# Kernel tuning notes

Hardware: AMD Instinct MI355X
Metric: run time of the kernel (lower is better)

## Reference

```python
import jax, jax.numpy as jnp
import numpy as np

N_NODES = 50000
N_EDGES = 400000
N_GRAPHS = 512
F = 32        # num_features
NB = 32       # mp_num_basis_fn
ZMAX = 118
CUTOFF = 5.0
NSPH = 9      # (mp_max_degree+1)^2 with max_degree=2
DEG_IDX = jnp.array([0, 1, 1, 1, 2, 2, 2, 2, 2])  # degree of each spherical component


def _bernstein(u, n=NB):
    # reciprocal_bernstein radial basis: Bernstein polynomials of degree n-1 at u in [0,1)
    k = jnp.arange(n, dtype=jnp.float32)
    log_binom = (jax.scipy.special.gammaln(float(n)) - jax.scipy.special.gammaln(k + 1.0)
                 - jax.scipy.special.gammaln(float(n) - k))
    u = jnp.clip(u, 1e-7, 1.0 - 1e-7)[..., None]
    return jnp.exp(log_binom + k * jnp.log(u) + (float(n) - 1.0 - k) * jnp.log1p(-u))


def _smooth_cutoff(r, cutoff=CUTOFF):
    t = r / cutoff
    return jnp.where(t < 1.0, jnp.exp(1.0 - 1.0 / jnp.clip(1.0 - t * t, 1e-7, None)), 0.0)


def _sph(u):
    # real spherical harmonics (cartesian normalization) up to degree 2; u: (E,3) unit vectors
    x, y, z = u[:, 0], u[:, 1], u[:, 2]
    c = jnp.sqrt(jnp.float32(3.0))
    return jnp.stack([jnp.ones_like(x), y, z, x,
                      c * x * y, c * y * z, 0.5 * (3.0 * z * z - 1.0),
                      c * z * x, 0.5 * c * (x * x - y * y)], axis=-1)


def _dense(x, W, b):
    # equivariant Dense: shared kernel over spherical components, bias only on scalar (l=0)
    y = jnp.einsum('nmf,fg->nmg', x, W)
    return y.at[:, 0, :].add(b)


def _silu_gate(x):
    # equivariant silu: scalar channel gates all degrees (scalar part -> exact silu)
    return x * jax.nn.sigmoid(x[:, 0:1, :])


def setup_inputs() -> dict:
    key = jax.random.key(0)
    ks = jax.random.split(key, 24)
    s = 1.0 / np.sqrt(F)
    sb = 1.0 / np.sqrt(NB)
    inp = {
        'positions': 2.0 * jax.random.normal(ks[0], (N_NODES, 3), jnp.float32),
        'embed': jax.random.normal(ks[1], (ZMAX, F), jnp.float32),
        'Wy0': sb * jax.random.normal(ks[2], (3, NB, F), jnp.float32),
        'Wx0': sb * jax.random.normal(ks[3], (3, NB, F), jnp.float32),
        'W1_0': s * jax.random.normal(ks[4], (F, F), jnp.float32),
        'b1_0': jnp.zeros((F,), jnp.float32),
        'W2_0': s * jax.random.normal(ks[5], (F, F), jnp.float32),
        'b2_0': jnp.zeros((F,), jnp.float32),
        'c0': jnp.full((1,), 0.5, jnp.float32),
        'Wr_last': sb * jax.random.normal(ks[6], (NB, F), jnp.float32),
        'W1_1': s * jax.random.normal(ks[7], (F, F), jnp.float32),
        'b1_1': jnp.zeros((F,), jnp.float32),
        'W2_1': s * jax.random.normal(ks[8], (F, F), jnp.float32),
        'b2_1': jnp.zeros((F,), jnp.float32),
        'c1': jnp.full((1,), 0.5, jnp.float32),
        'Wro1': s * jax.random.normal(ks[9], (F, F), jnp.float32),
        'bro1': jnp.zeros((F,), jnp.float32),
        'Wro2': s * jax.random.normal(ks[10], (F, 1), jnp.float32),
        'bro2': jnp.zeros((1,), jnp.float32),
        'atomic_bias': jax.random.normal(ks[11], (ZMAX,), jnp.float32),
        'atomic_numbers': jax.random.randint(ks[12], (N_NODES,), 0, ZMAX, jnp.int32),
        'dst_idx': jax.random.randint(ks[13], (N_EDGES,), 0, N_NODES, jnp.int32),
        'src_idx': jax.random.randint(ks[14], (N_EDGES,), 0, N_NODES, jnp.int32),
        'batch_segments': jnp.sort(jax.random.randint(ks[15], (N_NODES,), 0, N_GRAPHS, jnp.int32)),
        'graph_mask': jnp.ones((N_GRAPHS,), jnp.bool_),
    }
    return inp


def reference(positions, embed, Wy0, Wx0, W1_0, b1_0, W2_0, b2_0, c0,
              Wr_last, W1_1, b1_1, W2_1, b2_1, c1,
              Wro1, bro1, Wro2, bro2, atomic_bias,
              atomic_numbers, dst_idx, src_idx, batch_segments, graph_mask):
    # --- edge geometry (gather_src/gather_dst) ---
    disp = positions[src_idx] - positions[dst_idx]                # (E,3)
    r = jnp.sqrt(jnp.sum(disp * disp, axis=-1) + 1e-12)           # (E,)
    u = disp / r[:, None]
    Y = _sph(u)                                                   # (E,9)
    rbf = _bernstein(r / (r + 1.0)) * _smooth_cutoff(r)[:, None]  # (E,NB)

    # --- atomic embedding, lifted to (N, 9, F) with zero higher degrees ---
    x0 = embed[atomic_numbers]                                    # (N,F)
    x = jnp.concatenate([x0[:, None, :], jnp.zeros((N_NODES, NSPH - 1, F), x0.dtype)], axis=1)

    # --- iteration 0: full-degree equivariant message pass ---
    wy = jnp.einsum('eb,lbf->elf', rbf, Wy0)[:, DEG_IDX, :]       # (E,9,F) radial weights, (0,l)->l path
    wx = jnp.einsum('eb,lbf->elf', rbf, Wx0)[:, DEG_IDX, :]       # (l,0)->l path
    xs = x[src_idx]                                               # (E,9,F)
    msg = wy * Y[:, :, None] * xs[:, 0:1, :] + wx * xs
    y = jax.ops.segment_sum(msg, dst_idx, num_segments=N_NODES)   # (N,9,F)
    y = x + y
    y = _silu_gate(_dense(y, W1_0, b1_0))
    y = _dense(y, W2_0, b2_0)
    x = x + jax.nn.silu(c0) * y                                   # y_nl == 0 (era disabled)

    # --- iteration 1 (last): max_degree=0 message pass, then reduce to scalars ---
    w0 = rbf @ Wr_last                                            # (E,F)
    msg0 = w0 * x[src_idx, 0, :]
    y0 = jax.ops.segment_sum(msg0, dst_idx, num_segments=N_NODES) # (N,F)
    xs0 = x[:, 0, :]                                              # change_max_degree -> scalars
    y0 = xs0 + y0
    y0 = jax.nn.silu(y0 @ W1_1 + b1_1)
    y0 = y0 @ W2_1 + b2_1
    xs0 = xs0 + jax.nn.silu(c1) * y0

    # --- atomic readout and per-graph sum ---
    h = jax.nn.silu(xs0 @ Wro1 + bro1)
    e_atom = (h @ Wro2)[:, 0] + bro2[0] + atomic_bias[atomic_numbers]
    e_graph = jax.ops.segment_sum(e_atom, batch_segments, num_segments=N_GRAPHS)
    return jnp.where(graph_mask, e_graph, 0.0)
```

## Files before the change

### kernel.cpp

```cpp
#include <hip/hip_runtime.h>
#include <math.h>

#define NNODES 50000
#define NEDGES 400000
#define NGRAPHS 512
#define FDIM 32
#define CAP 32

#define NHALVES 4096
#define NPAIRS (NNODES / 2)
#define PQ   (NPAIRS / NHALVES)
#define PREM (NPAIRS % NHALVES)

static constexpr float BINOM31[32] = {
    1.f, 31.f, 465.f, 4495.f, 31465.f, 169911.f, 736281.f, 2629575.f,
    7888725.f, 20160075.f, 44352165.f, 84672315.f, 141120525.f, 206253075.f,
    265182525.f, 300540195.f, 300540195.f, 265182525.f, 206253075.f,
    141120525.f, 84672315.f, 44352165.f, 20160075.f, 7888725.f, 2629575.f,
    736281.f, 169911.f, 31465.f, 4495.f, 465.f, 31.f, 1.f
};

__device__ __forceinline__ float fast_rcp(float x) {
    return __builtin_amdgcn_rcpf(x);
}
__device__ __forceinline__ float silu(float x) {
    return x * fast_rcp(1.0f + __expf(-x));
}

__global__ __launch_bounds__(256) void build_csr(
    const float* __restrict__ pos,
    const int* __restrict__ srci, const int* __restrict__ dsti,
    const int* __restrict__ Z,
    float4* __restrict__ pay, int* __restrict__ deg,
    float* __restrict__ out)
{
    int e = blockIdx.x * 256 + threadIdx.x;
    if (e < NGRAPHS) out[e] = 0.0f;
    if (e >= NEDGES) return;
    int s = srci[e], d = dsti[e];
    float dx = pos[3 * s]     - pos[3 * d];
    float dy = pos[3 * s + 1] - pos[3 * d + 1];
    float dz = pos[3 * s + 2] - pos[3 * d + 2];
    float r = sqrtf(dx * dx + dy * dy + dz * dz + 1e-12f);
    if (r >= 5.0f) return;

    float t = r * 0.2f;
    float q = fmaxf(1.0f - t * t, 1e-7f);
    float cut = __expf(1.0f - fast_rcp(q));
    float v = fast_rcp(r + 1.0f);
    float v2 = v * v, v4 = v2 * v2, v8 = v4 * v4, v16 = v8 * v8;
    float scale = v16 * v8 * v4 * v2 * v * cut;

    int rank = atomicAdd(&deg[d], 1);
    if (rank < CAP)
        pay[(size_t)d * CAP + rank] =
            make_float4(r, scale,
                        __int_as_float(s * FDIM),
                        __int_as_float(Z[s] * FDIM));
}

#define GATHER4X2(ACCA, ACCB, XSRC, SEL)                                   \
    float ACCA = 0.0f, ACCB = 0.0f;                                        \
    {                                                                      \
        int _dm = max(dgA, dgB);                                           \
        for (int j = 0; j < _dm; j += 4) {                                 \
            float rrA[4], scA[4], xgA[4], hhA[4];                          \
            float rrB[4], scB[4], xgB[4], hhB[4];                          \
            _Pragma("unroll")                                              \
            for (int k = 0; k < 4; ++k) {                                  \
                float4 _pA = plA[j + k];                                   \
                float4 _pB = plB[j + k];                                   \
                rrA[k] = _pA.x; scA[k] = _pA.y;                            \
                rrB[k] = _pB.x; scB[k] = _pB.y;                            \
                xgA[k] = (XSRC)[__float_as_int(_pA.SEL) + f];              \
                xgB[k] = (XSRC)[__float_as_int(_pB.SEL) + f];              \
            }                                                              \
            _Pragma("unroll")                                              \
            for (int k = 0; k < 4; ++k) { hhA[k] = cw[31]; hhB[k] = cw[31]; } \
            _Pragma("unroll")                                              \
            for (int t = 30; t >= 0; --t) {                                \
                _Pragma("unroll")                                          \
                for (int k = 0; k < 4; ++k) {                              \
                    hhA[k] = fmaf(hhA[k], rrA[k], cw[t]);                  \
                    hhB[k] = fmaf(hhB[k], rrB[k], cw[t]);                  \
                }                                                          \
            }                                                              \
            _Pragma("unroll")                                              \
            for (int k = 0; k < 4; ++k) {                                  \
                ACCA = fmaf(scA[k] * hhA[k], xgA[k], ACCA);                \
                ACCB = fmaf(scB[k] * hhB[k], xgB[k], ACCB);                \
            }                                                              \
        }                                                                  \
    }

#define MV2C(AA, AB, WR, YPA, YPB, c)                                      \
    { float4 _qA = (YPA)[c]; float4 _qB = (YPB)[c];                        \
      AA = fmaf(_qA.x, WR[4*c],   AA); AB = fmaf(_qB.x, WR[4*c],   AB);    \
      AA = fmaf(_qA.y, WR[4*c+1], AA); AB = fmaf(_qB.y, WR[4*c+1], AB);    \
      AA = fmaf(_qA.z, WR[4*c+2], AA); AB = fmaf(_qB.z, WR[4*c+2], AB);    \
      AA = fmaf(_qA.w, WR[4*c+3], AA); AB = fmaf(_qB.w, WR[4*c+3], AB); }

#define MATVEC32R2(RA, RB, WR, BIAS, YPA, YPB) do {                        \
    float _aA0=(BIAS), _aA1=0.f, _aA2=0.f, _aA3=0.f;                       \
    float _aB0=(BIAS), _aB1=0.f, _aB2=0.f, _aB3=0.f;                       \
    MV2C(_aA0,_aB0,WR,YPA,YPB,0) MV2C(_aA1,_aB1,WR,YPA,YPB,1)              \
    MV2C(_aA2,_aB2,WR,YPA,YPB,2) MV2C(_aA3,_aB3,WR,YPA,YPB,3)              \
    MV2C(_aA0,_aB0,WR,YPA,YPB,4) MV2C(_aA1,_aB1,WR,YPA,YPB,5)              \
    MV2C(_aA2,_aB2,WR,YPA,YPB,6) MV2C(_aA3,_aB3,WR,YPA,YPB,7)              \
    RA = (_aA0+_aA1)+(_aA2+_aA3);                                          \
    RB = (_aB0+_aB1)+(_aB2+_aB3); } while (0)

__device__ __forceinline__ void pair_range(int h, int& p0, int& p1) {
    int a = h < PREM ? h * (PQ + 1) : PREM * (PQ + 1) + (h - PREM) * PQ;
    p0 = a;
    p1 = a + (h < PREM ? PQ + 1 : PQ);
}

__global__ __launch_bounds__(256, 2) void fused_a(
    const float4* __restrict__ pay, const int* __restrict__ deg,
    const float* __restrict__ embed, const int* __restrict__ Z,
    const float* __restrict__ Wy0, const float* __restrict__ Wx0,
    const float* __restrict__ W1, const float* __restrict__ b1,
    const float* __restrict__ W2, const float* __restrict__ b2,
    const float* __restrict__ c0,
    float* __restrict__ x1buf)
{
    __shared__ __align__(16) float ylds[4][2][2][FDIM];
    __shared__ __align__(16) float4 plds[4][2][2][CAP];
    int tid = threadIdx.x;
    int widx = tid >> 6;
    int lane = tid & 63;
    int f    = lane & 31;
    int half = lane >> 5;

    float cw[32], w1r[32], w2r[32];
    #pragma unroll
    for (int k = 0; k < 32; ++k) {
        cw[k]  = BINOM31[k] * (Wy0[k * FDIM + f] + Wx0[k * FDIM + f]);
        w1r[k] = W1[k * FDIM + f];
        w2r[k] = W2[k * FDIM + f];
    }
    float b1f = b1[f], b2f = b2[f];
    float sc0 = silu(c0[0]);

    int hidx = (blockIdx.x * 4 + widx) * 2 + half;
    int p0, p1;
    pair_range(hidx, p0, p1);

    float* yrA = &ylds[widx][half][0][0];
    float* yrB = &ylds[widx][half][1][0];
    const float4* ypA_ = (const float4*)yrA;
    const float4* ypB_ = (const float4*)yrB;
    float4* plA = &plds[widx][half][0][0];
    float4* plB = &plds[widx][half][1][0];

    int nA0 = 2 * p0, nB0 = nA0 + 1;
    int dgA = min(deg[nA0], CAP), dgB = min(deg[nB0], CAP);
    float4 pvA = make_float4(0.f, 0.f, 0.f, 0.f);
    float4 pvB = make_float4(0.f, 0.f, 0.f, 0.f);
    if (f < dgA) pvA = pay[(size_t)nA0 * CAP + f];
    if (f < dgB) pvB = pay[(size_t)nB0 * CAP + f];
    plA[f] = pvA;
    plB[f] = pvB;
    float x0A = embed[Z[nA0] * FDIM + f];
    float x0B = embed[Z[nB0] * FDIM + f];

    for (int p = p0; p < p1; ++p) {
        int nA = 2 * p, nB = nA + 1;
        int pn = (p + 1 < p1) ? p + 1 : p;
        int mA = 2 * pn, mB = mA + 1;
        int dgnA = min(deg[mA], CAP), dgnB = min(deg[mB], CAP);
        int znA = Z[mA], znB = Z[mB];
        float4 pvnA = make_float4(0.f, 0.f, 0.f, 0.f);
        float4 pvnB = make_float4(0.f, 0.f, 0.f, 0.f);
        if (f < dgnA) pvnA = pay[(size_t)mA * CAP + f];
        if (f < dgnB) pvnB = pay[(size_t)mB * CAP + f];

        GATHER4X2(accA, accB, embed, w)

        float x0nA = embed[znA * FDIM + f];
        float x0nB = embed[znB * FDIM + f];
        plA[f] = pvnA;
        plB[f] = pvnB;

        yrA[f] = x0A + accA;
        yrB[f] = x0B + accB;
        float tA, tB;
        MATVEC32R2(tA, tB, w1r, b1f, ypA_, ypB_);
        tA = silu(tA);
        tB = silu(tB);
        yrA[f] = tA;
        yrB[f] = tB;
        float uA, uB;
        MATVEC32R2(uA, uB, w2r, b2f, ypA_, ypB_);
        x1buf[(size_t)nA * FDIM + f] = fmaf(sc0, uA, x0A);
        x1buf[(size_t)nB * FDIM + f] = fmaf(sc0, uB, x0B);

        dgA = dgnA; dgB = dgnB; x0A = x0nA; x0B = x0nB;
    }
}

__global__ __launch_bounds__(256, 2) void fused_b(
    const float4* __restrict__ pay, const int* __restrict__ deg,
    const float* __restrict__ x1buf, const float* __restrict__ Wr_last,
    const float* __restrict__ W1, const float* __restrict__ b1,
    const float* __restrict__ W2, const float* __restrict__ b2,
    const float* __restrict__ c1,
    const float* __restrict__ Wro1, const float* __restrict__ bro1,
    const float* __restrict__ Wro2, const float* __restrict__ bro2,
    const float* __restrict__ abias, const int* __restrict__ Z,
    const int* __restrict__ segs,
    float* __restrict__ out)
{
    __shared__ __align__(16) float ylds[4][2][2][FDIM];
    __shared__ __align__(16) float4 plds[4][2][2][CAP];
    int tid = threadIdx.x;
    int widx = tid >> 6;
    int lane = tid & 63;
    int f    = lane & 31;
    int half = lane >> 5;

    float cw[32], w1r[32], w2r[32], wrr[32];
    #pragma unroll
    for (int k = 0; k < 32; ++k) {
        cw[k]  = BINOM31[k] * Wr_last[k * FDIM + f];
        w1r[k] = W1[k * FDIM + f];
        w2r[k] = W2[k * FDIM + f];
        wrr[k] = Wro1[k * FDIM + f];
    }
    float b1f = b1[f], b2f = b2[f], bro1f = bro1[f], wro2f = Wro2[f];
    float sc1 = silu(c1[0]);
    float bro2v = bro2[0];

    int hidx = (blockIdx.x * 4 + widx) * 2 + half;
    int p0, p1;
    pair_range(hidx, p0, p1);

    float* yrA = &ylds[widx][half][0][0];
    float* yrB = &ylds[widx][half][1][0];
    const float4* ypA_ = (const float4*)yrA;
    const float4* ypB_ = (const float4*)yrB;
    float4* plA = &plds[widx][half][0][0];
    float4* plB = &plds[widx][half][1][0];

    int nA0 = 2 * p0, nB0 = nA0 + 1;
    int dgA = min(deg[nA0], CAP), dgB = min(deg[nB0], CAP);
    float4 pvA = make_float4(0.f, 0.f, 0.f, 0.f);
    float4 pvB = make_float4(0.f, 0.f, 0.f, 0.f);
    if (f < dgA) pvA = pay[(size_t)nA0 * CAP + f];
    if (f < dgB) pvB = pay[(size_t)nB0 * CAP + f];
    plA[f] = pvA;
    plB[f] = pvB;
    float x1A = x1buf[(size_t)nA0 * FDIM + f];
    float x1B = x1buf[(size_t)nB0 * FDIM + f];
    float abA = abias[Z[nA0]], abB = abias[Z[nB0]];
    int   sgA = segs[nA0],     sgB = segs[nB0];

    float segacc = 0.0f;
    int   curseg = -1;

    for (int p = p0; p < p1; ++p) {
        int nA = 2 * p, nB = nA + 1;
        int pn = (p + 1 < p1) ? p + 1 : p;
        int mA = 2 * pn, mB = mA + 1;
        int dgnA = min(deg[mA], CAP), dgnB = min(deg[mB], CAP);
        int znA = Z[mA], znB = Z[mB];
        int sgnA = segs[mA], sgnB = segs[mB];
        float4 pvnA = make_float4(0.f, 0.f, 0.f, 0.f);
        float4 pvnB = make_float4(0.f, 0.f, 0.f, 0.f);
        if (f < dgnA) pvnA = pay[(size_t)mA * CAP + f];
        if (f < dgnB) pvnB = pay[(size_t)mB * CAP + f];

        GATHER4X2(accA, accB, x1buf, z)

        float x1nA = x1buf[(size_t)mA * FDIM + f];
        float x1nB = x1buf[(size_t)mB * FDIM + f];
        float abnA = abias[znA], abnB = abias[znB];
        plA[f] = pvnA;
        plB[f] = pvnB;

        yrA[f] = x1A + accA;
        yrB[f] = x1B + accB;
        float tA, tB;
        MATVEC32R2(tA, tB, w1r, b1f, ypA_, ypB_);
        tA = silu(tA);
        tB = silu(tB);
        yrA[f] = tA;
        yrB[f] = tB;
        float uA, uB;
        MATVEC32R2(uA, uB, w2r, b2f, ypA_, ypB_);
        float xsA = fmaf(sc1, uA, x1A);
        float xsB = fmaf(sc1, uB, x1B);
        yrA[f] = xsA;
        yrB[f] = xsB;
        float hA, hB;
        MATVEC32R2(hA, hB, wrr, bro1f, ypA_, ypB_);
        float pA = silu(hA) * wro2f;
        float pB = silu(hB) * wro2f;
        pA += __shfl_xor(pA, 16, 32); pB += __shfl_xor(pB, 16, 32);
        pA += __shfl_xor(pA, 8, 32);  pB += __shfl_xor(pB, 8, 32);
        pA += __shfl_xor(pA, 4, 32);  pB += __shfl_xor(pB, 4, 32);
        pA += __shfl_xor(pA, 2, 32);  pB += __shfl_xor(pB, 2, 32);
        pA += __shfl_xor(pA, 1, 32);  pB += __shfl_xor(pB, 1, 32);

        if (f == 0) {
            float eA = pA + bro2v + abA;
            if (sgA == curseg) segacc += eA;
            else {
                if (curseg >= 0) atomicAdd(&out[curseg], segacc);
                curseg = sgA; segacc = eA;
            }
            float eB = pB + bro2v + abB;
            if (sgB == curseg) segacc += eB;
            else {
                if (curseg >= 0) atomicAdd(&out[curseg], segacc);
                curseg = sgB; segacc = eB;
            }
        }

        dgA = dgnA; dgB = dgnB;
        x1A = x1nA; x1B = x1nB;
        abA = abnA; abB = abnB;
        sgA = sgnA; sgB = sgnB;
    }
    if (f == 0 && curseg >= 0) atomicAdd(&out[curseg], segacc);
}

extern "C" void kernel_launch(void* const* d_in, const int* in_sizes, int n_in,
                              void* d_out, int out_size, void* d_ws, size_t ws_size,
                              hipStream_t stream)
{
    const float* pos     = (const float*)d_in[0];
    const float* embed   = (const float*)d_in[1];
    const float* Wy0     = (const float*)d_in[2];
    const float* Wx0     = (const float*)d_in[3];
    const float* W1_0    = (const float*)d_in[4];
    const float* b1_0    = (const float*)d_in[5];
    const float* W2_0    = (const float*)d_in[6];
    const float* b2_0    = (const float*)d_in[7];
    const float* c0      = (const float*)d_in[8];
    const float* Wr_last = (const float*)d_in[9];
    const float* W1_1    = (const float*)d_in[10];
    const float* b1_1    = (const float*)d_in[11];
    const float* W2_1    = (const float*)d_in[12];
    const float* b2_1    = (const float*)d_in[13];
    const float* c1      = (const float*)d_in[14];
    const float* Wro1    = (const float*)d_in[15];
    const float* bro1    = (const float*)d_in[16];
    const float* Wro2    = (const float*)d_in[17];
    const float* bro2    = (const float*)d_in[18];
    const float* abias   = (const float*)d_in[19];
    const int*   Z       = (const int*)d_in[20];
    const int*   dsti    = (const int*)d_in[21];
    const int*   srci    = (const int*)d_in[22];
    const int*   segs    = (const int*)d_in[23];

    float* out = (float*)d_out;

    char* w = (char*)d_ws;
    float4* pay   = (float4*)w;  w += (size_t)NNODES * CAP * 16;
    float*  x1buf = (float*)w;   w += (size_t)NNODES * FDIM * 4;
    int*    deg   = (int*)w;     w += (size_t)NNODES * 4;

    const int edgeBlocks = (NEDGES + 255) / 256;
    const int persBlocks = NHALVES / 8;

    hipMemsetAsync(deg, 0, (size_t)NNODES * 4, stream);

    build_csr<<<edgeBlocks, 256, 0, stream>>>(pos, srci, dsti, Z, pay, deg, out);
    fused_a<<<persBlocks, 256, 0, stream>>>(pay, deg, embed, Z, Wy0, Wx0,
                                            W1_0, b1_0, W2_0, b2_0, c0, x1buf);
    fused_b<<<persBlocks, 256, 0, stream>>>(pay, deg, x1buf, Wr_last,
                                            W1_1, b1_1, W2_1, b2_1, c1,
                                            Wro1, bro1, Wro2, bro2,
                                            abias, Z, segs, out);
}
```

Measured before the change: 173.4 us.

## Process three nodes per half-wave and move W2/Wro1 weights to swizzled LDS

Each half-wave now handles three nodes per iteration instead of two, which exposes more independent gathers and polynomial evaluations for latency hiding. To make room in registers, the W2 and Wro1 weight matrices move from per-thread registers into shared memory using an XOR-swizzled column layout to avoid bank conflicts. Node partitioning switches from pairs to a per-node range with clamped tail handling. The cost is extra LDS traffic for the weights, one block-level sync, and duplicated work when the tail is padded.

```diff
diff --git a/kernel.cpp b/kernel.cpp
--- a/kernel.cpp
+++ b/kernel.cpp
@@ -8,9 +8,8 @@
 #define CAP 32
 
 #define NHALVES 4096
-#define NPAIRS (NNODES / 2)
-#define PQ   (NPAIRS / NHALVES)
-#define PREM (NPAIRS % NHALVES)
+#define NQ   (NNODES / NHALVES)
+#define NREM (NNODES % NHALVES)
 
 static constexpr float BINOM31[32] = {
     1.f, 31.f, 465.f, 4495.f, 31465.f, 169911.f, 736281.f, 2629575.f,
@@ -59,61 +58,109 @@
                         __int_as_float(Z[s] * FDIM));
 }
 
-#define GATHER4X2(ACCA, ACCB, XSRC, SEL)                                   \
-    float ACCA = 0.0f, ACCB = 0.0f;                                        \
+__device__ __forceinline__ int wcol_idx(int k, int f) {
+    return f * 64 + ((((k >> 2) ^ (f & 15))) << 2) + (k & 3);
+}
+
+#define GATHER4X3(ACCA, ACCB, ACCC, XSRC, SEL)                             \
+    float ACCA = 0.0f, ACCB = 0.0f, ACCC = 0.0f;                           \
     {                                                                      \
-        int _dm = max(dgA, dgB);                                           \
+        const float* XSRC_ = (XSRC);                                       \
+        int _dm = max(dgA, max(dgB, dgC));                                 \
         for (int j = 0; j < _dm; j += 4) {                                 \
             float rrA[4], scA[4], xgA[4], hhA[4];                          \
             float rrB[4], scB[4], xgB[4], hhB[4];                          \
+            float rrC[4], scC[4], xgC[4], hhC[4];                          \
             _Pragma("unroll")                                              \
             for (int k = 0; k < 4; ++k) {                                  \
-                float4 _pA = plA[j + k];                                   \
-                float4 _pB = plB[j + k];                                   \
+                float4 _pA = plA[j + k]; float4 _pB = plB[j + k];          \
+                float4 _pC = plC[j + k];                                   \
                 rrA[k] = _pA.x; scA[k] = _pA.y;                            \
                 rrB[k] = _pB.x; scB[k] = _pB.y;                            \
-                xgA[k] = (XSRC)[__float_as_int(_pA.SEL) + f];              \
-                xgB[k] = (XSRC)[__float_as_int(_pB.SEL) + f];              \
+                rrC[k] = _pC.x; scC[k] = _pC.y;                            \
+                xgA[k] = XSRC_[__float_as_int(_pA.SEL) + f];               \
+                xgB[k] = XSRC_[__float_as_int(_pB.SEL) + f];               \
+                xgC[k] = XSRC_[__float_as_int(_pC.SEL) + f];               \
             }                                                              \
             _Pragma("unroll")                                              \
-            for (int k = 0; k < 4; ++k) { hhA[k] = cw[31]; hhB[k] = cw[31]; } \
+            for (int k = 0; k < 4; ++k) {                                  \
+                hhA[k] = cw[31]; hhB[k] = cw[31]; hhC[k] = cw[31];         \
+            }                                                              \
             _Pragma("unroll")                                              \
             for (int t = 30; t >= 0; --t) {                                \
                 _Pragma("unroll")                                          \
                 for (int k = 0; k < 4; ++k) {                              \
                     hhA[k] = fmaf(hhA[k], rrA[k], cw[t]);                  \
                     hhB[k] = fmaf(hhB[k], rrB[k], cw[t]);                  \
+                    hhC[k] = fmaf(hhC[k], rrC[k], cw[t]);                  \
                 }                                                          \
             }                                                              \
             _Pragma("unroll")                                              \
             for (int k = 0; k < 4; ++k) {                                  \
                 ACCA = fmaf(scA[k] * hhA[k], xgA[k], ACCA);                \
                 ACCB = fmaf(scB[k] * hhB[k], xgB[k], ACCB);                \
+                ACCC = fmaf(scC[k] * hhC[k], xgC[k], ACCC);                \
             }                                                              \
         }                                                                  \
     }
 
-#define MV2C(AA, AB, WR, YPA, YPB, c)                                      \
-    { float4 _qA = (YPA)[c]; float4 _qB = (YPB)[c];                        \
+#define MV3C(AA, AB, AC, WR, c)                                            \
+    { float4 _qA = ypA_[c]; float4 _qB = ypB_[c]; float4 _qC = ypC_[c];    \
       AA = fmaf(_qA.x, WR[4*c],   AA); AB = fmaf(_qB.x, WR[4*c],   AB);    \
+      AC = fmaf(_qC.x, WR[4*c],   AC);                                     \
       AA = fmaf(_qA.y, WR[4*c+1], AA); AB = fmaf(_qB.y, WR[4*c+1], AB);    \
+      AC = fmaf(_qC.y, WR[4*c+1], AC);                                     \
       AA = fmaf(_qA.z, WR[4*c+2], AA); AB = fmaf(_qB.z, WR[4*c+2], AB);    \
-      AA = fmaf(_qA.w, WR[4*c+3], AA); AB = fmaf(_qB.w, WR[4*c+3], AB); }
-
-#define MATVEC32R2(RA, RB, WR, BIAS, YPA, YPB) do {                        \
+      AC = fmaf(_qC.z, WR[4*c+2], AC);                                     \
+      AA = fmaf(_qA.w, WR[4*c+3], AA); AB = fmaf(_qB.w, WR[4*c+3], AB);    \
+      AC = fmaf(_qC.w, WR[4*c+3], AC); }
+
+#define MATVEC32R3(RA, RB, RC, WR, BIAS) do {                              \
     float _aA0=(BIAS), _aA1=0.f, _aA2=0.f, _aA3=0.f;                       \
     float _aB0=(BIAS), _aB1=0.f, _aB2=0.f, _aB3=0.f;                       \
-    MV2C(_aA0,_aB0,WR,YPA,YPB,0) MV2C(_aA1,_aB1,WR,YPA,YPB,1)              \
-    MV2C(_aA2,_aB2,WR,YPA,YPB,2) MV2C(_aA3,_aB3,WR,YPA,YPB,3)              \
-    MV2C(_aA0,_aB0,WR,YPA,YPB,4) MV2C(_aA1,_aB1,WR,YPA,YPB,5)              \
-    MV2C(_aA2,_aB2,WR,YPA,YPB,6) MV2C(_aA3,_aB3,WR,YPA,YPB,7)              \
+    float _aC0=(BIAS), _aC1=0.f, _aC2=0.f, _aC3=0.f;                       \
+    MV3C(_aA0,_aB0,_aC0,WR,0) MV3C(_aA1,_aB1,_aC1,WR,1)                    \
+    MV3C(_aA2,_aB2,_aC2,WR,2) MV3C(_aA3,_aB3,_aC3,WR,3)                    \
+    MV3C(_aA0,_aB0,_aC0,WR,4) MV3C(_aA1,_aB1,_aC1,WR,5)                    \
+    MV3C(_aA2,_aB2,_aC2,WR,6) MV3C(_aA3,_aB3,_aC3,WR,7)                    \
     RA = (_aA0+_aA1)+(_aA2+_aA3);                                          \
-    RB = (_aB0+_aB1)+(_aB2+_aB3); } while (0)
-
-__device__ __forceinline__ void pair_range(int h, int& p0, int& p1) {
-    int a = h < PREM ? h * (PQ + 1) : PREM * (PQ + 1) + (h - PREM) * PQ;
-    p0 = a;
-    p1 = a + (h < PREM ? PQ + 1 : PQ);
+    RB = (_aB0+_aB1)+(_aB2+_aB3);                                          \
+    RC = (_aC0+_aC1)+(_aC2+_aC3); } while (0)
+
+#define MATVEC32C3(RA, RB, RC, WC, BIAS) do {                              \
+    const float4* _w4 = (const float4*)(WC);                               \
+    float _aA0=(BIAS), _aA1=0.f, _aA2=0.f, _aA3=0.f;                       \
+    float _aB0=(BIAS), _aB1=0.f, _aB2=0.f, _aB3=0.f;                       \
+    float _aC0=(BIAS), _aC1=0.f, _aC2=0.f, _aC3=0.f;                       \
+    _Pragma("unroll")                                                      \
+    for (int c = 0; c < 8; ++c) {                                          \
+        float4 _wc = _w4[(f << 4) + (c ^ (f & 15))];                       \
+        float4 _qA = ypA_[c]; float4 _qB = ypB_[c]; float4 _qC = ypC_[c];  \
+        float _sA = fmaf(_qA.x, _wc.x, 0.f);                               \
+        _sA = fmaf(_qA.y, _wc.y, _sA);                                     \
+        _sA = fmaf(_qA.z, _wc.z, _sA);                                     \
+        _sA = fmaf(_qA.w, _wc.w, _sA);                                     \
+        float _sB = fmaf(_qB.x, _wc.x, 0.f);                               \
+        _sB = fmaf(_qB.y, _wc.y, _sB);                                     \
+        _sB = fmaf(_qB.z, _wc.z, _sB);                                     \
+        _sB = fmaf(_qB.w, _wc.w, _sB);                                     \
+        float _sC = fmaf(_qC.x, _wc.x, 0.f);                               \
+        _sC = fmaf(_qC.y, _wc.y, _sC);                                     \
+        _sC = fmaf(_qC.z, _wc.z, _sC);                                     \
+        _sC = fmaf(_qC.w, _wc.w, _sC);                                     \
+        if ((c & 3) == 0)      { _aA0 += _sA; _aB0 += _sB; _aC0 += _sC; }  \
+        else if ((c & 3) == 1) { _aA1 += _sA; _aB1 += _sB; _aC1 += _sC; }  \
+        else if ((c & 3) == 2) { _aA2 += _sA; _aB2 += _sB; _aC2 += _sC; }  \
+        else                   { _aA3 += _sA; _aB3 += _sB; _aC3 += _sC; }  \
+    }                                                                      \
+    RA = (_aA0+_aA1)+(_aA2+_aA3);                                          \
+    RB = (_aB0+_aB1)+(_aB2+_aB3);                                          \
+    RC = (_aC0+_aC1)+(_aC2+_aC3); } while (0)
+
+__device__ __forceinline__ void half_range(int h, int& n0, int& n1) {
+    int a = h < NREM ? h * (NQ + 1) : NREM * (NQ + 1) + (h - NREM) * NQ;
+    n0 = a;
+    n1 = a + (h < NREM ? NQ + 1 : NQ);
 }
 
 __global__ __launch_bounds__(256, 2) void fused_a(
@@ -125,78 +172,101 @@
     const float* __restrict__ c0,
     float* __restrict__ x1buf)
 {
-    __shared__ __align__(16) float ylds[4][2][2][FDIM];
-    __shared__ __align__(16) float4 plds[4][2][2][CAP];
+    __shared__ __align__(16) float ylds[4][2][3][FDIM];
+    __shared__ __align__(16) float4 plds[4][2][3][CAP];
+    __shared__ __align__(16) float w2c[FDIM * 64];
     int tid = threadIdx.x;
     int widx = tid >> 6;
     int lane = tid & 63;
     int f    = lane & 31;
     int half = lane >> 5;
 
-    float cw[32], w1r[32], w2r[32];
+    float cw[32], w1r[32];
     #pragma unroll
     for (int k = 0; k < 32; ++k) {
         cw[k]  = BINOM31[k] * (Wy0[k * FDIM + f] + Wx0[k * FDIM + f]);
         w1r[k] = W1[k * FDIM + f];
-        w2r[k] = W2[k * FDIM + f];
+    }
+    for (int i = tid; i < FDIM * FDIM; i += 256) {
+        int k = i >> 5, ff = i & 31;
+        w2c[wcol_idx(k, ff)] = W2[i];
     }
     float b1f = b1[f], b2f = b2[f];
     float sc0 = silu(c0[0]);
+    __syncthreads();
 
     int hidx = (blockIdx.x * 4 + widx) * 2 + half;
-    int p0, p1;
-    pair_range(hidx, p0, p1);
+    int n0, n1;
+    half_range(hidx, n0, n1);
 
     float* yrA = &ylds[widx][half][0][0];
     float* yrB = &ylds[widx][half][1][0];
+    float* yrC = &ylds[widx][half][2][0];
     const float4* ypA_ = (const float4*)yrA;
     const float4* ypB_ = (const float4*)yrB;
+    const float4* ypC_ = (const float4*)yrC;
     float4* plA = &plds[widx][half][0][0];
     float4* plB = &plds[widx][half][1][0];
-
-    int nA0 = 2 * p0, nB0 = nA0 + 1;
-    int dgA = min(deg[nA0], CAP), dgB = min(deg[nB0], CAP);
-    float4 pvA = make_float4(0.f, 0.f, 0.f, 0.f);
-    float4 pvB = make_float4(0.f, 0.f, 0.f, 0.f);
-    if (f < dgA) pvA = pay[(size_t)nA0 * CAP + f];
-    if (f < dgB) pvB = pay[(size_t)nB0 * CAP + f];
-    plA[f] = pvA;
-    plB[f] = pvB;
-    float x0A = embed[Z[nA0] * FDIM + f];
-    float x0B = embed[Z[nB0] * FDIM + f];
-
-    for (int p = p0; p < p1; ++p) {
-        int nA = 2 * p, nB = nA + 1;
-        int pn = (p + 1 < p1) ? p + 1 : p;
-        int mA = 2 * pn, mB = mA + 1;
-        int dgnA = min(deg[mA], CAP), dgnB = min(deg[mB], CAP);
-        int znA = Z[mA], znB = Z[mB];
-        float4 pvnA = make_float4(0.f, 0.f, 0.f, 0.f);
-        float4 pvnB = make_float4(0.f, 0.f, 0.f, 0.f);
-        if (f < dgnA) pvnA = pay[(size_t)mA * CAP + f];
+    float4* plC = &plds[widx][half][2][0];
+
+    int cA = n0;
+    int cB = (n0 + 1 < n1) ? n0 + 1 : n1 - 1;
+    int cC = (n0 + 2 < n1) ? n0 + 2 : n1 - 1;
+    int dgA = min(deg[cA], CAP), dgB = min(deg[cB], CAP),
+        dgC = min(deg[cC], CAP);
+    {
+        float4 z4 = make_float4(0.f, 0.f, 0.f, 0.f);
+        float4 pA = z4, pB = z4, pC = z4;
+        if (f < dgA) pA = pay[(size_t)cA * CAP + f];
+        if (f < dgB) pB = pay[(size_t)cB * CAP + f];
+        if (f < dgC) pC = pay[(size_t)cC * CAP + f];
+        plA[f] = pA; plB[f] = pB; plC[f] = pC;
+    }
+    float x0A = embed[Z[cA] * FDIM + f];
+    float x0B = embed[Z[cB] * FDIM + f];
+    float x0C = embed[Z[cC] * FDIM + f];
+
+    for (int n = n0; n < n1; n += 3) {
+        int curA = n;
+        int curB = (n + 1 < n1) ? n + 1 : n1 - 1;
+        int curC = (n + 2 < n1) ? n + 2 : n1 - 1;
+        int m  = (n + 3 < n1) ? n + 3 : n;
+        int mB = (m + 1 < n1) ? m + 1 : n1 - 1;
+        int mC = (m + 2 < n1) ? m + 2 : n1 - 1;
+        int dgnA = min(deg[m],  CAP);
+        int dgnB = min(deg[mB], CAP);
+        int dgnC = min(deg[mC], CAP);
+        int znA = Z[m], znB = Z[mB], znC = Z[mC];
+        float4 z4 = make_float4(0.f, 0.f, 0.f, 0.f);
+        float4 pvnA = z4, pvnB = z4, pvnC = z4;
+        if (f < dgnA) pvnA = pay[(size_t)m  * CAP + f];
         if (f < dgnB) pvnB = pay[(size_t)mB * CAP + f];
-
-        GATHER4X2(accA, accB, embed, w)
+        if (f < dgnC) pvnC = pay[(size_t)mC * CAP + f];
+
+        GATHER4X3(accA, accB, accC, embed, w)
 
         float x0nA = embed[znA * FDIM + f];
         float x0nB = embed[znB * FDIM + f];
+        float x0nC = embed[znC * FDIM + f];
         plA[f] = pvnA;
         plB[f] = pvnB;
+        plC[f] = pvnC;
 
         yrA[f] = x0A + accA;
         yrB[f] = x0B + accB;
-        float tA, tB;
-        MATVEC32R2(tA, tB, w1r, b1f, ypA_, ypB_);
-        tA = silu(tA);
-        tB = silu(tB);
-        yrA[f] = tA;
-        yrB[f] = tB;
-        float uA, uB;
-        MATVEC32R2(uA, uB, w2r, b2f, ypA_, ypB_);
-        x1buf[(size_t)nA * FDIM + f] = fmaf(sc0, uA, x0A);
-        x1buf[(size_t)nB * FDIM + f] = fmaf(sc0, uB, x0B);
-
-        dgA = dgnA; dgB = dgnB; x0A = x0nA; x0B = x0nB;
+        yrC[f] = x0C + accC;
+        float tA, tB, tC;
+        MATVEC32R3(tA, tB, tC, w1r, b1f);
+        tA = silu(tA); tB = silu(tB); tC = silu(tC);
+        yrA[f] = tA; yrB[f] = tB; yrC[f] = tC;
+        float uA, uB, uC;
+        MATVEC32C3(uA, uB, uC, w2c, b2f);
+        x1buf[(size_t)curA * FDIM + f] = fmaf(sc0, uA, x0A);
+        x1buf[(size_t)curB * FDIM + f] = fmaf(sc0, uB, x0B);
+        x1buf[(size_t)curC * FDIM + f] = fmaf(sc0, uC, x0C);
+
+        dgA = dgnA; dgB = dgnB; dgC = dgnC;
+        x0A = x0nA; x0B = x0nB; x0C = x0nC;
     }
 }
 
@@ -212,116 +282,147 @@
     const int* __restrict__ segs,
     float* __restrict__ out)
 {
-    __shared__ __align__(16) float ylds[4][2][2][FDIM];
-    __shared__ __align__(16) float4 plds[4][2][2][CAP];
+    __shared__ __align__(16) float ylds[4][2][3][FDIM];
+    __shared__ __align__(16) float4 plds[4][2][3][CAP];
+    __shared__ __align__(16) float w2c[FDIM * 64];
+    __shared__ __align__(16) float wrc[FDIM * 64];
     int tid = threadIdx.x;
     int widx = tid >> 6;
     int lane = tid & 63;
     int f    = lane & 31;
     int half = lane >> 5;
 
-    float cw[32], w1r[32], w2r[32], wrr[32];
+    float cw[32], w1r[32];
     #pragma unroll
     for (int k = 0; k < 32; ++k) {
         cw[k]  = BINOM31[k] * Wr_last[k * FDIM + f];
         w1r[k] = W1[k * FDIM + f];
-        w2r[k] = W2[k * FDIM + f];
-        wrr[k] = Wro1[k * FDIM + f];
+    }
+    for (int i = tid; i < FDIM * FDIM; i += 256) {
+        int k = i >> 5, ff = i & 31;
+        w2c[wcol_idx(k, ff)] = W2[i];
+        wrc[wcol_idx(k, ff)] = Wro1[i];
     }
     float b1f = b1[f], b2f = b2[f], bro1f = bro1[f], wro2f = Wro2[f];
     float sc1 = silu(c1[0]);
     float bro2v = bro2[0];
+    __syncthreads();
 
     int hidx = (blockIdx.x * 4 + widx) * 2 + half;
-    int p0, p1;
-    pair_range(hidx, p0, p1);
+    int n0, n1;
+    half_range(hidx, n0, n1);
 
     float* yrA = &ylds[widx][half][0][0];
     float* yrB = &ylds[widx][half][1][0];
+    float* yrC = &ylds[widx][half][2][0];
     const float4* ypA_ = (const float4*)yrA;
     const float4* ypB_ = (const float4*)yrB;
+    const float4* ypC_ = (const float4*)yrC;
     float4* plA = &plds[widx][half][0][0];
     float4* plB = &plds[widx][half][1][0];
-
-    int nA0 = 2 * p0, nB0 = nA0 + 1;
-    int dgA = min(deg[nA0], CAP), dgB = min(deg[nB0], CAP);
-    float4 pvA = make_float4(0.f, 0.f, 0.f, 0.f);
-    float4 pvB = make_float4(0.f, 0.f, 0.f, 0.f);
-    if (f < dgA) pvA = pay[(size_t)nA0 * CAP + f];
-    if (f < dgB) pvB = pay[(size_t)nB0 * CAP + f];
-    plA[f] = pvA;
-    plB[f] = pvB;
-    float x1A = x1buf[(size_t)nA0 * FDIM + f];
-    float x1B = x1buf[(size_t)nB0 * FDIM + f];
-    float abA = abias[Z[nA0]], abB = abias[Z[nB0]];
-    int   sgA = segs[nA0],     sgB = segs[nB0];
+    float4* plC = &plds[widx][half][2][0];
+
+    int cA = n0;
+    int cB = (n0 + 1 < n1) ? n0 + 1 : n1 - 1;
+    int cC = (n0 + 2 < n1) ? n0 + 2 : n1 - 1;
+    int dgA = min(deg[cA], CAP), dgB = min(deg[cB], CAP),
+        dgC = min(deg[cC], CAP);
+    {
+        float4 z4 = make_float4(0.f, 0.f, 0.f, 0.f);
+        float4 pA = z4, pB = z4, pC = z4;
+        if (f < dgA) pA = pay[(size_t)cA * CAP + f];
+        if (f < dgB) pB = pay[(size_t)cB * CAP + f];
+        if (f < dgC) pC = pay[(size_t)cC * CAP + f];
+        plA[f] = pA; plB[f] = pB; plC[f] = pC;
+    }
+    float x1A = x1buf[(size_t)cA * FDIM + f];
+    float x1B = x1buf[(size_t)cB * FDIM + f];
+    float x1C = x1buf[(size_t)cC * FDIM + f];
+    float abA = abias[Z[cA]], abB = abias[Z[cB]], abC = abias[Z[cC]];
+    int   sgA = segs[cA],     sgB = segs[cB],     sgC = segs[cC];
 
     float segacc = 0.0f;
     int   curseg = -1;
 
-    for (int p = p0; p < p1; ++p) {
-        int nA = 2 * p, nB = nA + 1;
-        int pn = (p + 1 < p1) ? p + 1 : p;
-        int mA = 2 * pn, mB = mA + 1;
-        int dgnA = min(deg[mA], CAP), dgnB = min(deg[mB], CAP);
-        int znA = Z[mA], znB = Z[mB];
-        int sgnA = segs[mA], sgnB = segs[mB];
-        float4 pvnA = make_float4(0.f, 0.f, 0.f, 0.f);
-        float4 pvnB = make_float4(0.f, 0.f, 0.f, 0.f);
-        if (f < dgnA) pvnA = pay[(size_t)mA * CAP + f];
+    for (int n = n0; n < n1; n += 3) {
+        bool vB = (n + 1 < n1);
+        bool vC = (n + 2 < n1);
+        int m  = (n + 3 < n1) ? n + 3 : n;
+        int mB = (m + 1 < n1) ? m + 1 : n1 - 1;
+        int mC = (m + 2 < n1) ? m + 2 : n1 - 1;
+        int dgnA = min(deg[m],  CAP);
+        int dgnB = min(deg[mB], CAP);
+        int dgnC = min(deg[mC], CAP);
+        int znA = Z[m], znB = Z[mB], znC = Z[mC];
+        int sgnA = segs[m], sgnB = segs[mB], sgnC = segs[mC];
+        float4 z4 = make_float4(0.f, 0.f, 0.f, 0.f);
+        float4 pvnA = z4, pvnB = z4, pvnC = z4;
+        if (f < dgnA) pvnA = pay[(size_t)m  * CAP + f];
         if (f < dgnB) pvnB = pay[(size_t)mB * CAP + f];
-
-        GATHER4X2(accA, accB, x1buf, z)
-
-        float x1nA = x1buf[(size_t)mA * FDIM + f];
+        if (f < dgnC) pvnC = pay[(size_t)mC * CAP + f];
+
+        GATHER4X3(accA, accB, accC, x1buf, z)
+
+        float x1nA = x1buf[(size_t)m  * FDIM + f];
         float x1nB = x1buf[(size_t)mB * FDIM + f];
-        float abnA = abias[znA], abnB = abias[znB];
+        float x1nC = x1buf[(size_t)mC * FDIM + f];
+        float abnA = abias[znA], abnB = abias[znB], abnC = abias[znC];
         plA[f] = pvnA;
         plB[f] = pvnB;
+        plC[f] = pvnC;
 
         yrA[f] = x1A + accA;
         yrB[f] = x1B + accB;
-        float tA, tB;
-        MATVEC32R2(tA, tB, w1r, b1f, ypA_, ypB_);
-        tA = silu(tA);
-        tB = silu(tB);
-        yrA[f] = tA;
-        yrB[f] = tB;
-        float uA, uB;
-        MATVEC32R2(uA, uB, w2r, b2f, ypA_, ypB_);
+        yrC[f] = x1C + accC;
+        float tA, tB, tC;
+        MATVEC32R3(tA, tB, tC, w1r, b1f);
+        tA = silu(tA); tB = silu(tB); tC = silu(tC);
+        yrA[f] = tA; yrB[f] = tB; yrC[f] = tC;
+        float uA, uB, uC;
+        MATVEC32C3(uA, uB, uC, w2c, b2f);
         float xsA = fmaf(sc1, uA, x1A);
         float xsB = fmaf(sc1, uB, x1B);
-        yrA[f] = xsA;
-        yrB[f] = xsB;
-        float hA, hB;
-        MATVEC32R2(hA, hB, wrr, bro1f, ypA_, ypB_);
+        float xsC = fmaf(sc1, uC, x1C);
+        yrA[f] = xsA; yrB[f] = xsB; yrC[f] = xsC;
+        float hA, hB, hC;
+        MATVEC32C3(hA, hB, hC, wrc, bro1f);
         float pA = silu(hA) * wro2f;
         float pB = silu(hB) * wro2f;
+        float pC = silu(hC) * wro2f;
         pA += __shfl_xor(pA, 16, 32); pB += __shfl_xor(pB, 16, 32);
+        pC += __shfl_xor(pC, 16, 32);
         pA += __shfl_xor(pA, 8, 32);  pB += __shfl_xor(pB, 8, 32);
+        pC += __shfl_xor(pC, 8, 32);
         pA += __shfl_xor(pA, 4, 32);  pB += __shfl_xor(pB, 4, 32);
+        pC += __shfl_xor(pC, 4, 32);
         pA += __shfl_xor(pA, 2, 32);  pB += __shfl_xor(pB, 2, 32);
+        pC += __shfl_xor(pC, 2, 32);
         pA += __shfl_xor(pA, 1, 32);  pB += __shfl_xor(pB, 1, 32);
+        pC += __shfl_xor(pC, 1, 32);
 
         if (f == 0) {
             float eA = pA + bro2v + abA;
             if (sgA == curseg) segacc += eA;
-            else {
-                if (curseg >= 0) atomicAdd(&out[curseg], segacc);
-                curseg = sgA; segacc = eA;
+            else { if (curseg >= 0) atomicAdd(&out[curseg], segacc);
+                   curseg = sgA; segacc = eA; }
+            if (vB) {
+                float eB = pB + bro2v + abB;
+                if (sgB == curseg) segacc += eB;
+                else { if (curseg >= 0) atomicAdd(&out[curseg], segacc);
+                       curseg = sgB; segacc = eB; }
             }
-            float eB = pB + bro2v + abB;
-            if (sgB == curseg) segacc += eB;
-            else {
-                if (curseg >= 0) atomicAdd(&out[curseg], segacc);
-                curseg = sgB; segacc = eB;
+            if (vC) {
+                float eC = pC + bro2v + abC;
+                if (sgC == curseg) segacc += eC;
+                else { if (curseg >= 0) atomicAdd(&out[curseg], segacc);
+                       curseg = sgC; segacc = eC; }
             }
         }
 
-        dgA = dgnA; dgB = dgnB;
-        x1A = x1nA; x1B = x1nB;
-        abA = abnA; abB = abnB;
-        sgA = sgnA; sgB = sgnB;
+        dgA = dgnA; dgB = dgnB; dgC = dgnC;
+        x1A = x1nA; x1B = x1nB; x1C = x1nC;
+        abA = abnA; abB = abnB; abC = abnC;
+        sgA = sgnA; sgB = sgnB; sgC = sgnC;
     }
     if (f == 0 && curseg >= 0) atomicAdd(&out[curseg], segacc);
 }
```

After: 183.8 us. 6.0% more time.
